# Performance work log

Hardware: AMD Instinct MI355X
Metric: run time of the kernel (lower is better)

## Reference

```python
import jax, jax.numpy as jnp
import numpy as np

N = 100000          # nodes
E = 1600000         # edges (avg degree 16)
D_IN = 128          # in_features
D_OUT = 128         # out_features


def setup_inputs() -> dict:
    key = jax.random.key(0)
    k1, k2, k3, k4 = jax.random.split(key, 4)
    H = jax.random.normal(k1, (N, D_IN), dtype=jnp.float32)
    # COO indices of sparse adjacency A: row i aggregates features of col j
    src = jax.random.randint(k2, (E,), 0, N, dtype=jnp.int32)
    dst = jax.random.randint(k3, (E,), 0, N, dtype=jnp.int32)
    # nn.Linear(2*in_features, out_features): weight [out, 2*in], zero bias
    W = jax.random.normal(k4, (D_OUT, 2 * D_IN), dtype=jnp.float32) * 0.05
    b = jnp.zeros((D_OUT,), dtype=jnp.float32)
    return {"H": H, "src": src, "dst": dst, "W": W, "b": b}


def reference(H, src, dst, W, b):
    # max-aggregation: for each node i, max over features of its neighbors.
    # One fused gather + segment-max replaces the per-node Python loop.
    gathered = H[dst]  # [E, D_IN]
    agg = jax.ops.segment_max(gathered, src, num_segments=N)  # [N, D_IN]
    # nodes with no incoming edges stay zero (torch code leaves zeros)
    deg = jax.ops.segment_sum(jnp.ones((src.shape[0],), jnp.float32), src,
                              num_segments=N)  # [N]
    H_neigh = jnp.where(deg[:, None] > 0, agg, 0.0)
    H_concat = jnp.concatenate([H, H_neigh], axis=1)  # [N, 2*D_IN]
    return H_concat @ W.T + b
```

## Files before the change

kernel.cpp:

```cpp
#include <hip/hip_runtime.h>
#include <math.h>

#define NN 100000
#define NE 1600000
#define DD 128
#define NB 782
#define CAP 2432
#define PB 196
#define CB 392
#define XP 72

#define WS_HH  0
#define WS_CUR 6400000
#define WS_ENT (WS_CUR + NB)
#define WS_AH  (WS_ENT + NB * CAP)
#define WS_WH  (WS_AH + NN * (DD / 2))

typedef __attribute__((ext_vector_type(8))) _Float16 h8_t;
typedef __attribute__((ext_vector_type(4))) _Float16 h4_t;
typedef __attribute__((ext_vector_type(2))) _Float16 h2_t;
typedef __attribute__((ext_vector_type(4))) float f4_t;

__device__ __forceinline__ unsigned pk2h(float x, float y) {
    h2_t h;
    h.x = (_Float16)x;
    h.y = (_Float16)y;
    return *(unsigned*)&h;
}

__device__ __forceinline__ h4_t h4max(h4_t a, h4_t b) {
    return __builtin_elementwise_max(a, b);
}

__global__ __launch_bounds__(1024) void prep_kernel(const float* __restrict__ H,
                                                    const int* __restrict__ src,
                                                    const int* __restrict__ dst,
                                                    int* __restrict__ cursor,
                                                    unsigned* __restrict__ entries,
                                                    uint4* __restrict__ Hh4,
                                                    const float* __restrict__ W,
                                                    unsigned* __restrict__ Wh) {
    __shared__ int cnt[NB];
    __shared__ int gcur[NB];
    const int t = threadIdx.x;
    const int b = blockIdx.x;
    if (b < PB) {
        for (int i = t; i < NB; i += 1024) cnt[i] = 0;
        __syncthreads();
        const int base = b * 8192;
        int sv[8];
#pragma unroll
        for (int k = 0; k < 8; ++k) {
            int e = base + k * 1024 + t;
            sv[k] = (e < NE) ? src[e] : -1;
            if (sv[k] >= 0) atomicAdd(&cnt[sv[k] >> 7], 1);
        }
        __syncthreads();
        for (int i = t; i < NB; i += 1024) {
            int c = cnt[i];
            gcur[i] = c ? i * CAP + atomicAdd(&cursor[i], c) : 0;
        }
        __syncthreads();
#pragma unroll
        for (int k = 0; k < 8; ++k) {
            int e = base + k * 1024 + t;
            if (sv[k] >= 0) {
                int s = sv[k];
                int pos = atomicAdd(&gcur[s >> 7], 1);
                entries[pos] = ((unsigned)(s & 127) << 17) | (unsigned)dst[e];
            }
        }
    } else if (b < PB + CB) {
        const int nb = b - PB;
        const int n8 = NN * DD / 8;
        for (int i = nb * 1024 + t; i < n8; i += CB * 1024) {
            const float4* s = (const float4*)H + (size_t)i * 2;
            float4 a = s[0], c4 = s[1];
            uint4 o;
            o.x = pk2h(a.x, a.y);
            o.y = pk2h(a.z, a.w);
            o.z = pk2h(c4.x, c4.y);
            o.w = pk2h(c4.z, c4.w);
            Hh4[i] = o;
        }
    } else {
        for (int i = t; i < 128 * 256 / 2; i += 1024)
            Wh[i] = pk2h(W[2 * i], W[2 * i + 1]);
    }
}

__global__ __launch_bounds__(512) void agg_kernel(const _Float16* __restrict__ Hh,
                                                  const int* __restrict__ cursor,
                                                  const unsigned* __restrict__ entries,
                                                  unsigned* __restrict__ Ah) {
    __shared__ unsigned raw[CAP];
    __shared__ unsigned sorted[CAP];
    __shared__ int cnt[128], base_s[128], cur[128];
    const int t = threadIdx.x;
    const int b = blockIdx.x;
    const int n = cursor[b];

    if (t < 128) cnt[t] = 0;
    __syncthreads();
    for (int i = t; i < n; i += 512) {
        unsigned e = entries[b * CAP + i];
        raw[i] = e;
        atomicAdd(&cnt[e >> 17], 1);
    }
    __syncthreads();
    if (t < 64) {
        int v0 = cnt[2 * t], v1 = cnt[2 * t + 1];
        int s = v0 + v1;
        int incl = s;
#pragma unroll
        for (int o = 1; o < 64; o <<= 1) {
            int y = __shfl_up(incl, o, 64);
            if (t >= o) incl += y;
        }
        int excl = incl - s;
        base_s[2 * t] = excl;
        cur[2 * t] = excl;
        base_s[2 * t + 1] = excl + v0;
        cur[2 * t + 1] = excl + v0;
    }
    __syncthreads();
    for (int i = t; i < n; i += 512) {
        unsigned e = raw[i];
        int pos = atomicAdd(&cur[e >> 17], 1);
        sorted[pos] = e & 0x1FFFFu;
    }
    __syncthreads();

    const int lane = t & 63;
    const int w = t >> 6;
    const int half = lane >> 5;
    const int l32 = lane & 31;
    const _Float16* __restrict__ colbase = Hh + l32 * 4;
#pragma unroll
    for (int q = 0; q < 16; ++q) {
        int ln = w * 16 + q;
        int s0 = base_s[ln];
        int e0 = s0 + cnt[ln];
        unsigned long long mu = 0xFC00FC00FC00FC00ull;
        h4_t m = *(h4_t*)&mu;
        int j = s0 + half;
        for (; j + 6 < e0; j += 8) {
            int d0 = sorted[j], d1 = sorted[j + 2];
            int d2 = sorted[j + 4], d3 = sorted[j + 6];
            h4_t v0 = *(const h4_t*)(colbase + (size_t)d0 * DD);
            h4_t v1 = *(const h4_t*)(colbase + (size_t)d1 * DD);
            h4_t v2 = *(const h4_t*)(colbase + (size_t)d2 * DD);
            h4_t v3 = *(const h4_t*)(colbase + (size_t)d3 * DD);
            m = h4max(m, h4max(h4max(v0, v1), h4max(v2, v3)));
        }
        for (; j < e0; j += 2) {
            h4_t v0 = *(const h4_t*)(colbase + (size_t)sorted[j] * DD);
            m = h4max(m, v0);
        }
        uint2 mv = *(uint2*)&m;
        uint2 ov;
        ov.x = (unsigned)__shfl_xor((int)mv.x, 32, 64);
        ov.y = (unsigned)__shfl_xor((int)mv.y, 32, 64);
        h4_t om = *(h4_t*)&ov;
        m = h4max(m, om);
        int node = b * 128 + ln;
        if (half == 0 && node < NN) {
            uint2 outv = make_uint2(0u, 0u);
            if (s0 < e0) outv = *(uint2*)&m;
            *(uint2*)(Ah + (size_t)node * 64 + l32 * 2) = outv;
        }
    }
}

__global__ __launch_bounds__(512) void mfma_direct_kernel(
        const unsigned short* __restrict__ Hh,
        const unsigned short* __restrict__ Ah,
        const unsigned short* __restrict__ Wh,
        const float* __restrict__ bias,
        float* __restrict__ out) {
    __shared__ unsigned short Ws[128 * XP];
    const int t = threadIdx.x;
    const int lane = t & 63;
    const int w = t >> 6;
    const int quad = lane >> 4;
    const int l16 = lane & 15;
    const int arow = blockIdx.x * 128 + w * 16 + l16;
    const bool aok = arow < NN;

    f4_t acc[8] = {};
#pragma unroll
    for (int c = 0; c < 4; ++c) {
        __syncthreads();
        {
            const int seg = t & 7, o0 = t >> 3;
#pragma unroll
            for (int j = 0; j < 2; ++j) {
                int o = o0 + 64 * j;
                *(uint4*)&Ws[o * XP + seg * 8] =
                    *(const uint4*)(Wh + (size_t)o * 256 + c * 64 + seg * 8);
            }
        }
        __syncthreads();
        const unsigned short* xb = (c < 2) ? Hh : Ah;
        const int koff = (c & 1) * 64;
#pragma unroll
        for (int kk = 0; kk < 64; kk += 32) {
            uint4 av = make_uint4(0, 0, 0, 0);
            if (aok)
                av = *(const uint4*)(xb + (size_t)arow * DD + koff + kk + quad * 8);
            h8_t a = *(h8_t*)&av;
#pragma unroll
            for (int ot = 0; ot < 8; ++ot) {
                h8_t bf = *(const h8_t*)&Ws[(ot * 16 + l16) * XP + kk + quad * 8];
                acc[ot] = __builtin_amdgcn_mfma_f32_16x16x32_f16(a, bf, acc[ot], 0, 0, 0);
            }
        }
    }

#pragma unroll
    for (int ot = 0; ot < 8; ++ot) {
        float bv = bias[ot * 16 + l16];
#pragma unroll
        for (int reg = 0; reg < 4; ++reg) {
            int row = blockIdx.x * 128 + w * 16 + quad * 4 + reg;
            if (row < NN)
                out[(size_t)row * DD + ot * 16 + l16] = acc[ot][reg] + bv;
        }
    }
}

extern "C" void kernel_launch(void* const* d_in, const int* in_sizes, int n_in,
                              void* d_out, int out_size, void* d_ws, size_t ws_size,
                              hipStream_t stream) {
    const float* H   = (const float*)d_in[0];
    const int*   src = (const int*)d_in[1];
    const int*   dst = (const int*)d_in[2];
    const float* W   = (const float*)d_in[3];
    const float* b   = (const float*)d_in[4];
    float* out = (float*)d_out;

    int* ws = (int*)d_ws;
    unsigned short* Hh      = (unsigned short*)(ws + WS_HH);
    int*            cursor  = ws + WS_CUR;
    unsigned*       entries = (unsigned*)(ws + WS_ENT);
    unsigned*       Ah      = (unsigned*)(ws + WS_AH);
    unsigned short* Wh      = (unsigned short*)(ws + WS_WH);

    hipMemsetAsync(cursor, 0, NB * sizeof(int), stream);
    prep_kernel<<<PB + CB + 1, 1024, 0, stream>>>(H, src, dst, cursor, entries,
                                                  (uint4*)Hh, W, (unsigned*)Wh);
    agg_kernel<<<NB, 512, 0, stream>>>((const _Float16*)Hh, cursor, entries, Ah);
    mfma_direct_kernel<<<(NN + 127) / 128, 512, 0, stream>>>(
        Hh, (const unsigned short*)Ah, Wh, b, out);
}
```

Measured before the change: 221.3 us.

## Split aggregation into sort and column-sliced gather kernels with dst-partitioned passes

The fused bucket-sort-plus-gather kernel becomes two kernels. A sort kernel counting-sorts each bin's edges by source node and also by the top bits of the destination index, then writes the sorted entries and per-subbucket start offsets back to global memory. A gather kernel launches four blocks per bin, each handling a 32-column slice. It runs two passes over destination-range halves so that each pass touches a smaller portion of H, aiming for better cache locality and more parallelism. The cost is an extra kernel launch, a global round-trip for the sorted entries, and narrower 8-byte gathers per edge with more shuffle reductions.

New measurement: 359.2 us. 1.62x slower.

```diff
diff --git a/kernel.cpp b/kernel.cpp
--- a/kernel.cpp
+++ b/kernel.cpp
@@ -15,6 +15,7 @@
 #define WS_ENT (WS_CUR + NB)
 #define WS_AH  (WS_ENT + NB * CAP)
 #define WS_WH  (WS_AH + NN * (DD / 2))
+#define WS_ST  (WS_WH + 16384)
 
 typedef __attribute__((ext_vector_type(8))) _Float16 h8_t;
 typedef __attribute__((ext_vector_type(4))) _Float16 h4_t;
@@ -89,85 +90,128 @@
     }
 }
 
-__global__ __launch_bounds__(512) void agg_kernel(const _Float16* __restrict__ Hh,
-                                                  const int* __restrict__ cursor,
-                                                  const unsigned* __restrict__ entries,
-                                                  unsigned* __restrict__ Ah) {
+__global__ __launch_bounds__(512) void sort_kernel(const int* __restrict__ cursor,
+                                                   unsigned* __restrict__ entries,
+                                                   unsigned short* __restrict__ starts) {
     __shared__ unsigned raw[CAP];
-    __shared__ unsigned sorted[CAP];
-    __shared__ int cnt[128], base_s[128], cur[128];
+    __shared__ int cnt[512], base_s[512], cur[512];
     const int t = threadIdx.x;
     const int b = blockIdx.x;
     const int n = cursor[b];
 
-    if (t < 128) cnt[t] = 0;
+    if (t < 512) cnt[t] = 0;
     __syncthreads();
     for (int i = t; i < n; i += 512) {
         unsigned e = entries[b * CAP + i];
         raw[i] = e;
-        atomicAdd(&cnt[e >> 17], 1);
+        int key = (int)((e >> 17) << 2) | (int)((e & 0x1FFFFu) >> 15);
+        atomicAdd(&cnt[key], 1);
     }
     __syncthreads();
     if (t < 64) {
-        int v0 = cnt[2 * t], v1 = cnt[2 * t + 1];
-        int s = v0 + v1;
+        int v[8];
+        int s = 0;
+#pragma unroll
+        for (int k = 0; k < 8; ++k) { v[k] = cnt[t * 8 + k]; s += v[k]; }
         int incl = s;
 #pragma unroll
         for (int o = 1; o < 64; o <<= 1) {
             int y = __shfl_up(incl, o, 64);
             if (t >= o) incl += y;
         }
-        int excl = incl - s;
-        base_s[2 * t] = excl;
-        cur[2 * t] = excl;
-        base_s[2 * t + 1] = excl + v0;
-        cur[2 * t + 1] = excl + v0;
+        int run = incl - s;
+#pragma unroll
+        for (int k = 0; k < 8; ++k) {
+            base_s[t * 8 + k] = run;
+            cur[t * 8 + k] = run;
+            run += v[k];
+        }
     }
     __syncthreads();
     for (int i = t; i < n; i += 512) {
         unsigned e = raw[i];
-        int pos = atomicAdd(&cur[e >> 17], 1);
-        sorted[pos] = e & 0x1FFFFu;
-    }
+        int key = (int)((e >> 17) << 2) | (int)((e & 0x1FFFFu) >> 15);
+        int pos = atomicAdd(&cur[key], 1);
+        entries[b * CAP + pos] = e & 0x1FFFFu;
+    }
+    for (int i = t; i < 512; i += 512)
+        starts[b * 512 + i] = (unsigned short)base_s[i];
+}
+
+__global__ __launch_bounds__(256) void gather_kernel(
+        const _Float16* __restrict__ Hh,
+        const int* __restrict__ cursor,
+        const unsigned* __restrict__ sorted,
+        const unsigned short* __restrict__ starts,
+        unsigned* __restrict__ Ah) {
+    __shared__ unsigned short st[513];
+    __shared__ unsigned pm[128][16];
+    const int t = threadIdx.x;
+    const int bin = blockIdx.x >> 2;
+    const int slice = blockIdx.x & 3;
+    const int n = cursor[bin];
+
+    st[t] = starts[bin * 512 + t];
+    st[t + 256] = starts[bin * 512 + 256 + t];
+    if (t == 0) st[512] = (unsigned short)n;
     __syncthreads();
 
     const int lane = t & 63;
     const int w = t >> 6;
-    const int half = lane >> 5;
-    const int l32 = lane & 31;
-    const _Float16* __restrict__ colbase = Hh + l32 * 4;
-#pragma unroll
-    for (int q = 0; q < 16; ++q) {
-        int ln = w * 16 + q;
-        int s0 = base_s[ln];
-        int e0 = s0 + cnt[ln];
-        unsigned long long mu = 0xFC00FC00FC00FC00ull;
-        h4_t m = *(h4_t*)&mu;
-        int j = s0 + half;
-        for (; j + 6 < e0; j += 8) {
-            int d0 = sorted[j], d1 = sorted[j + 2];
-            int d2 = sorted[j + 4], d3 = sorted[j + 6];
-            h4_t v0 = *(const h4_t*)(colbase + (size_t)d0 * DD);
-            h4_t v1 = *(const h4_t*)(colbase + (size_t)d1 * DD);
-            h4_t v2 = *(const h4_t*)(colbase + (size_t)d2 * DD);
-            h4_t v3 = *(const h4_t*)(colbase + (size_t)d3 * DD);
-            m = h4max(m, h4max(h4max(v0, v1), h4max(v2, v3)));
-        }
-        for (; j < e0; j += 2) {
-            h4_t v0 = *(const h4_t*)(colbase + (size_t)sorted[j] * DD);
-            m = h4max(m, v0);
-        }
-        uint2 mv = *(uint2*)&m;
-        uint2 ov;
-        ov.x = (unsigned)__shfl_xor((int)mv.x, 32, 64);
-        ov.y = (unsigned)__shfl_xor((int)mv.y, 32, 64);
-        h4_t om = *(h4_t*)&ov;
-        m = h4max(m, om);
-        int node = b * 128 + ln;
-        if (half == 0 && node < NN) {
-            uint2 outv = make_uint2(0u, 0u);
-            if (s0 < e0) outv = *(uint2*)&m;
-            *(uint2*)(Ah + (size_t)node * 64 + l32 * 2) = outv;
+    const int g = lane >> 3;
+    const int c = lane & 7;
+    const _Float16* __restrict__ colbase = Hh + slice * 32 + c * 4;
+    const unsigned* __restrict__ sbin = sorted + (size_t)bin * CAP;
+
+#pragma unroll
+    for (int p = 0; p < 2; ++p) {
+        for (int ni = 0; ni < 32; ++ni) {
+            const int node = w * 32 + ni;
+            const int qsel = 2 * p + (g >> 2);
+            const int kb = node * 4 + qsel;
+            const int s0 = st[kb];
+            const int e0 = st[kb + 1];
+            h4_t m;
+            if (p == 0) {
+                unsigned long long mu = 0xFC00FC00FC00FC00ull;
+                m = *(h4_t*)&mu;
+            } else {
+                uint2 pv;
+                pv.x = pm[node][c * 2];
+                pv.y = pm[node][c * 2 + 1];
+                m = *(h4_t*)&pv;
+            }
+            for (int j = s0 + (g & 3); j < e0; j += 4) {
+                int d = sbin[j];
+                h4_t v = *(const h4_t*)(colbase + (size_t)d * DD);
+                m = h4max(m, v);
+            }
+            uint2 mv = *(uint2*)&m;
+#pragma unroll
+            for (int mask = 8; mask <= 32; mask <<= 1) {
+                uint2 ov;
+                ov.x = (unsigned)__shfl_xor((int)mv.x, mask, 64);
+                ov.y = (unsigned)__shfl_xor((int)mv.y, mask, 64);
+                h4_t a = *(h4_t*)&mv;
+                h4_t o = *(h4_t*)&ov;
+                a = h4max(a, o);
+                mv = *(uint2*)&a;
+            }
+            if (g == 0) {
+                pm[node][c * 2] = mv.x;
+                pm[node][c * 2 + 1] = mv.y;
+            }
+        }
+        __syncthreads();
+    }
+
+    for (int i = t; i < 128 * 16; i += 256) {
+        int node = i >> 4, ci = i & 15;
+        int gnode = bin * 128 + node;
+        if (gnode < NN) {
+            int deg = (int)st[node * 4 + 4] - (int)st[node * 4];
+            unsigned v = (deg > 0) ? pm[node][ci] : 0u;
+            Ah[(size_t)gnode * 64 + slice * 16 + ci] = v;
         }
     }
 }
@@ -245,11 +289,14 @@
     unsigned*       entries = (unsigned*)(ws + WS_ENT);
     unsigned*       Ah      = (unsigned*)(ws + WS_AH);
     unsigned short* Wh      = (unsigned short*)(ws + WS_WH);
+    unsigned short* starts  = (unsigned short*)(ws + WS_ST);
 
     hipMemsetAsync(cursor, 0, NB * sizeof(int), stream);
     prep_kernel<<<PB + CB + 1, 1024, 0, stream>>>(H, src, dst, cursor, entries,
                                                   (uint4*)Hh, W, (unsigned*)Wh);
-    agg_kernel<<<NB, 512, 0, stream>>>((const _Float16*)Hh, cursor, entries, Ah);
+    sort_kernel<<<NB, 512, 0, stream>>>(cursor, entries, starts);
+    gather_kernel<<<NB * 4, 256, 0, stream>>>((const _Float16*)Hh, cursor,
+                                              entries, starts, Ah);
     mfma_direct_kernel<<<(NN + 127) / 128, 512, 0, stream>>>(
         Hh, (const unsigned short*)Ah, Wh, b, out);
 }
```
